# Performance work log

Hardware: AMD Instinct MI355X
Metric: run time of the kernel (lower is better)

Reference implementation:

```python
import jax, jax.numpy as jnp
import numpy as np

B, L = 8, 128            # batch, max_length
VF = 32128               # full (padded) T5 vocab in logits
V = 32100                # act_vocab_size (codebook entries)
D = 768                  # embed_dim
TAU = 1.0                # gumbel-softmax temperature
EPS = 1e-8               # cosine-similarity eps (torch default)


def setup_inputs() -> dict:
    key = jax.random.key(0)
    k1, k2, k3, k4, k5 = jax.random.split(key, 5)
    logits = jax.random.normal(k1, (B, L, VF), jnp.float32)
    u = jax.random.uniform(k2, (B, L, VF), jnp.float32, 1e-6, 1.0 - 1e-6)
    gumbel_noise = -jnp.log(-jnp.log(u))
    word_embeddings = jax.random.normal(k3, (V, D), jnp.float32) * 0.02
    # rewrite attention mask: ones prefix of random length per row
    lengths = jax.random.randint(k4, (B,), 1, L)
    rwrt_attention = (jnp.arange(L)[None, :] < lengths[:, None]).astype(jnp.int32)
    psg_input = jax.random.randint(k5, (B, L), 0, V)
    # mimic torch.roll(psg_input, 1, 1); psg_input[:, 0] = 1
    psg_input = jnp.roll(psg_input, 1, axis=1).at[:, 0].set(1)
    return dict(logits=logits, gumbel_noise=gumbel_noise,
                word_embeddings=word_embeddings,
                rwrt_attention=rwrt_attention, psg_input=psg_input)


def reference(logits, gumbel_noise, word_embeddings, rwrt_attention, psg_input):
    # --- hard gumbel-softmax (straight-through) ---
    y = jax.nn.softmax((logits + gumbel_noise) / TAU, axis=-1)      # [B,L,VF]
    hard = jax.nn.one_hot(jnp.argmax(y, axis=-1), VF, dtype=y.dtype)
    g = hard + y - jax.lax.stop_gradient(y)
    g = g[..., :V]                                                   # [B,L,V]

    # --- soft codebook lookup (one-hot @ embedding table) ---
    embeds = jnp.einsum('blv,vd->bld', g, word_embeddings)           # [B,L,D]
    embeds = embeds * rwrt_attention.astype(embeds.dtype)[:, :, None]

    # --- passage extraction + per-row roll-by-gather ---
    flipped = jnp.fliplr(rwrt_attention)
    keep = 1 - flipped
    extr = (keep.astype(psg_input.dtype)) * psg_input                # [B,L]
    shifts = jnp.sum(rwrt_attention == 1, axis=1)                    # [B]
    pos = jnp.arange(L)
    src = (pos[None, :] - shifts[:, None]) % L                       # right-roll
    idx = jnp.take_along_axis(extr, src, axis=1)                     # [B,L]

    # flag-gated embedding lookup: skip leading zeros, then always gather
    flag = jnp.cumsum((idx != 0).astype(jnp.int32), axis=1) > 0      # [B,L]
    psg_emb = jnp.where(flag[:, :, None], word_embeddings[idx], 0.0)
    embeds = embeds + psg_emb                                        # [B,L,D]

    # --- brute-force cosine-similarity NN decode over the codebook ---
    rn = embeds / jnp.maximum(jnp.linalg.norm(embeds, axis=-1, keepdims=True), EPS)
    wn = word_embeddings / jnp.maximum(
        jnp.linalg.norm(word_embeddings, axis=-1, keepdims=True), EPS)
    sims = jnp.einsum('bld,vd->blv', rn, wn)                         # [B,L,V]
    nn_idx = jnp.argmax(sims, axis=-1)                               # [B,L]
    return embeds, nn_idx
```

## Files before the change

kernel.cpp:

```cpp
#include <hip/hip_runtime.h>
#include <math.h>
#include <limits.h>

#define B_  8
#define L_  128
#define VF_ 32128
#define V_  32100
#define D_  768

typedef unsigned long long u64;

__device__ __forceinline__ unsigned int fmap(float f) {
    unsigned int u = __float_as_uint(f);
    return (u & 0x80000000u) ? ~u : (u | 0x80000000u);
}

__global__ __launch_bounds__(512) void k_argmax(
    const float* __restrict__ logits, const float* __restrict__ gumbel,
    u64* __restrict__ keys)
{
    const int row = blockIdx.x;
    const int tid = threadIdx.x;
    const float4* lp = (const float4*)(logits + (size_t)row * VF_);
    const float4* gp = (const float4*)(gumbel + (size_t)row * VF_);
    const int NV4 = VF_ / 4;

    float bv0 = -INFINITY, bv1 = -INFINITY, bv2 = -INFINITY, bv3 = -INFINITY;
    int   bi0 = 0, bi1 = 0, bi2 = 0, bi3 = 0;

#define UPD(A, G, I, BV, BI)                                              \
    { float v;                                                            \
      v = (A).x + (G).x; if (v > (BV)) { (BV) = v; (BI) = 4*(I) + 0; }    \
      v = (A).y + (G).y; if (v > (BV)) { (BV) = v; (BI) = 4*(I) + 1; }    \
      v = (A).z + (G).z; if (v > (BV)) { (BV) = v; (BI) = 4*(I) + 2; }    \
      v = (A).w + (G).w; if (v > (BV)) { (BV) = v; (BI) = 4*(I) + 3; } }

#pragma unroll
    for (int p = 0; p < 4; ++p) {
        const int i0 = p * 2048 + tid;
        const int i1 = i0 + 512;
        const int i2 = i0 + 1024;
        const int i3 = i0 + 1536;
        const bool ok3 = (i3 < NV4);
        float4 A0 = lp[i0], G0 = gp[i0];
        float4 A1 = lp[i1], G1 = gp[i1];
        float4 A2 = lp[i2], G2 = gp[i2];
        float4 A3, G3;
        if (ok3) { A3 = lp[i3]; G3 = gp[i3]; }
        UPD(A0, G0, i0, bv0, bi0)
        UPD(A1, G1, i1, bv1, bi1)
        UPD(A2, G2, i2, bv2, bi2)
        if (ok3) UPD(A3, G3, i3, bv3, bi3)
    }
#undef UPD

    u64 k0 = ((u64)fmap(bv0) << 32) | (u64)(VF_ - bi0);
    u64 k1 = ((u64)fmap(bv1) << 32) | (u64)(VF_ - bi1);
    u64 k2 = ((u64)fmap(bv2) << 32) | (u64)(VF_ - bi2);
    u64 k3 = ((u64)fmap(bv3) << 32) | (u64)(VF_ - bi3);
    u64 k = k0; if (k1 > k) k = k1; if (k2 > k) k = k2; if (k3 > k) k = k3;

    for (int off = 32; off > 0; off >>= 1) {
        u64 o = __shfl_down(k, off, 64);
        if (o > k) k = o;
    }
    if ((tid & 63) == 0) atomicMax(keys + row, k);
}

__global__ __launch_bounds__(128) void k_rowsel(
    const int* __restrict__ rwrt, const int* __restrict__ psg,
    const u64* __restrict__ keys,
    int* __restrict__ rowA, int* __restrict__ rowB,
    float* __restrict__ nn_out)
{
    const int b = blockIdx.x;
    const int l = threadIdx.x;

    __shared__ int s_att[L_];
    __shared__ int s_extr[L_];
    __shared__ int s_len;
    __shared__ int s_first;

    const int att = rwrt[b * L_ + l];
    s_att[l] = att;
    if (l == 0) s_first = INT_MAX;
    __syncthreads();

    if (l == 0) {
        int len = 0;
        for (int i = 0; i < L_; ++i) len += (s_att[i] == 1);
        s_len = len;
    }
    const int keep = 1 - s_att[L_ - 1 - l];
    s_extr[l] = keep * psg[b * L_ + l];
    __syncthreads();

    const int len  = s_len;
    const int src  = (l - len + L_) & (L_ - 1);
    const int idxv = s_extr[src];
    if (idxv != 0) atomicMin(&s_first, l);
    __syncthreads();

    const int flag = (l >= s_first) ? 1 : 0;
    const int am   = VF_ - (int)(keys[b * L_ + l] & 0xFFFFFFFFull);
    const int rA   = (att == 1 && am < V_) ? am : -1;
    const int rB   = flag ? idxv : -1;
    rowA[b * L_ + l] = rA;
    rowB[b * L_ + l] = rB;

    int nn = (rA >= 0) ? rA : ((rB >= 0) ? rB : 0);
    nn_out[b * L_ + l] = (float)nn;
}

__global__ __launch_bounds__(192) void k_gather(
    const float* __restrict__ W,
    const int* __restrict__ rowA, const int* __restrict__ rowB,
    float* __restrict__ out)
{
    const int row = blockIdx.x;
    const int t   = threadIdx.x;
    const int rA = rowA[row];
    const int rB = rowB[row];
    float4 v = make_float4(0.f, 0.f, 0.f, 0.f);
    if (rA >= 0) {
        float4 a = ((const float4*)(W + (size_t)rA * D_))[t];
        v.x += a.x; v.y += a.y; v.z += a.z; v.w += a.w;
    }
    if (rB >= 0) {
        float4 a = ((const float4*)(W + (size_t)rB * D_))[t];
        v.x += a.x; v.y += a.y; v.z += a.z; v.w += a.w;
    }
    ((float4*)(out + (size_t)row * D_))[t] = v;
}

extern "C" void kernel_launch(void* const* d_in, const int* in_sizes, int n_in,
                              void* d_out, int out_size, void* d_ws, size_t ws_size,
                              hipStream_t stream)
{
    const float* logits = (const float*)d_in[0];
    const float* gumbel = (const float*)d_in[1];
    const float* W      = (const float*)d_in[2];
    const int*   rwrt   = (const int*)d_in[3];
    const int*   psg    = (const int*)d_in[4];

    float* out    = (float*)d_out;
    float* nn_out = out + (size_t)B_ * L_ * D_;

    u64* keys = (u64*)d_ws;
    int* rowA = (int*)(keys + B_ * L_);
    int* rowB = rowA + B_ * L_;

    hipMemsetAsync(keys, 0, B_ * L_ * sizeof(u64), stream);
    k_argmax<<<B_ * L_, 512, 0, stream>>>(logits, gumbel, keys);
    k_rowsel<<<B_, L_, 0, stream>>>(rwrt, psg, keys, rowA, rowB, nn_out);
    k_gather<<<B_ * L_, 192, 0, stream>>>(W, rowA, rowB, out);
}
```

Before: 324.1 us.

## Split argmax rows into eight segments across more, smaller blocks

The argmax kernel now splits each logits row into 8 segments of 1024 float4s. Each segment is handled by its own 256-thread block that issues all loads up front and merges through atomicMax. This raises the block count from 1024 to 8192 and the occupancy hint, aiming to put more memory requests in flight and better saturate HBM bandwidth on the 264 MB streaming read. It costs more atomics per row and a single serial max chain per thread instead of four independent ones.

New measurement: 321.6 us. About the same (-0.8%).

```diff
diff --git a/kernel.cpp b/kernel.cpp
--- a/kernel.cpp
+++ b/kernel.cpp
@@ -8,6 +8,10 @@
 #define V_  32100
 #define D_  768
 
+#define SEGS_   8
+#define SEGF4_  1024
+#define NV4_    (VF_ / 4)
+
 typedef unsigned long long u64;
 
 __device__ __forceinline__ unsigned int fmap(float f) {
@@ -15,51 +19,49 @@
     return (u & 0x80000000u) ? ~u : (u | 0x80000000u);
 }
 
-__global__ __launch_bounds__(512) void k_argmax(
+__global__ __launch_bounds__(256, 8) void k_argmax(
     const float* __restrict__ logits, const float* __restrict__ gumbel,
     u64* __restrict__ keys)
 {
-    const int row = blockIdx.x;
+    const int row = blockIdx.x >> 3;
+    const int seg = blockIdx.x & 7;
     const int tid = threadIdx.x;
-    const float4* lp = (const float4*)(logits + (size_t)row * VF_);
-    const float4* gp = (const float4*)(gumbel + (size_t)row * VF_);
-    const int NV4 = VF_ / 4;
+    const size_t rowoff = (size_t)row * VF_;
+    const float4* lp = (const float4*)(logits + rowoff);
+    const float4* gp = (const float4*)(gumbel + rowoff);
+    const int base = seg * SEGF4_ + tid;
 
-    float bv0 = -INFINITY, bv1 = -INFINITY, bv2 = -INFINITY, bv3 = -INFINITY;
-    int   bi0 = 0, bi1 = 0, bi2 = 0, bi3 = 0;
+    float bv = -INFINITY;
+    int   bi = 0;
 
-#define UPD(A, G, I, BV, BI)                                              \
-    { float v;                                                            \
-      v = (A).x + (G).x; if (v > (BV)) { (BV) = v; (BI) = 4*(I) + 0; }    \
-      v = (A).y + (G).y; if (v > (BV)) { (BV) = v; (BI) = 4*(I) + 1; }    \
-      v = (A).z + (G).z; if (v > (BV)) { (BV) = v; (BI) = 4*(I) + 2; }    \
-      v = (A).w + (G).w; if (v > (BV)) { (BV) = v; (BI) = 4*(I) + 3; } }
+    const int i0 = base;
+    const int i1 = base + 256;
+    const int i2 = base + 512;
+    const int i3 = base + 768;
+    const bool k0 = (i0 < NV4_);
+    const bool k1 = (i1 < NV4_);
+    const bool k2 = (i2 < NV4_);
+    const bool k3 = (i3 < NV4_);
 
-#pragma unroll
-    for (int p = 0; p < 4; ++p) {
-        const int i0 = p * 2048 + tid;
-        const int i1 = i0 + 512;
-        const int i2 = i0 + 1024;
-        const int i3 = i0 + 1536;
-        const bool ok3 = (i3 < NV4);
-        float4 A0 = lp[i0], G0 = gp[i0];
-        float4 A1 = lp[i1], G1 = gp[i1];
-        float4 A2 = lp[i2], G2 = gp[i2];
-        float4 A3, G3;
-        if (ok3) { A3 = lp[i3]; G3 = gp[i3]; }
-        UPD(A0, G0, i0, bv0, bi0)
-        UPD(A1, G1, i1, bv1, bi1)
-        UPD(A2, G2, i2, bv2, bi2)
-        if (ok3) UPD(A3, G3, i3, bv3, bi3)
-    }
+    float4 A0, A1, A2, A3, G0, G1, G2, G3;
+    if (k0) { A0 = lp[i0]; G0 = gp[i0]; }
+    if (k1) { A1 = lp[i1]; G1 = gp[i1]; }
+    if (k2) { A2 = lp[i2]; G2 = gp[i2]; }
+    if (k3) { A3 = lp[i3]; G3 = gp[i3]; }
+
+#define UPD(A, G, I)                                                  \
+    { float v;                                                        \
+      v = (A).x + (G).x; if (v > bv) { bv = v; bi = 4*(I) + 0; }      \
+      v = (A).y + (G).y; if (v > bv) { bv = v; bi = 4*(I) + 1; }      \
+      v = (A).z + (G).z; if (v > bv) { bv = v; bi = 4*(I) + 2; }      \
+      v = (A).w + (G).w; if (v > bv) { bv = v; bi = 4*(I) + 3; } }
+    if (k0) UPD(A0, G0, i0)
+    if (k1) UPD(A1, G1, i1)
+    if (k2) UPD(A2, G2, i2)
+    if (k3) UPD(A3, G3, i3)
 #undef UPD
 
-    u64 k0 = ((u64)fmap(bv0) << 32) | (u64)(VF_ - bi0);
-    u64 k1 = ((u64)fmap(bv1) << 32) | (u64)(VF_ - bi1);
-    u64 k2 = ((u64)fmap(bv2) << 32) | (u64)(VF_ - bi2);
-    u64 k3 = ((u64)fmap(bv3) << 32) | (u64)(VF_ - bi3);
-    u64 k = k0; if (k1 > k) k = k1; if (k2 > k) k = k2; if (k3 > k) k = k3;
-
+    u64 k = ((u64)fmap(bv) << 32) | (u64)(VF_ - bi);
     for (int off = 32; off > 0; off >>= 1) {
         u64 o = __shfl_down(k, off, 64);
         if (o > k) k = o;
@@ -151,7 +153,7 @@
     int* rowB = rowA + B_ * L_;
 
     hipMemsetAsync(keys, 0, B_ * L_ * sizeof(u64), stream);
-    k_argmax<<<B_ * L_, 512, 0, stream>>>(logits, gumbel, keys);
+    k_argmax<<<B_ * L_ * SEGS_, 256, 0, stream>>>(logits, gumbel, keys);
     k_rowsel<<<B_, L_, 0, stream>>>(rwrt, psg, keys, rowA, rowB, nn_out);
     k_gather<<<B_ * L_, 192, 0, stream>>>(W, rowA, rowB, out);
 }
```
